# Kernel optimization log

Measured on AMD Instinct MI355X. Metric: run time of the kernel, lower is better.

## Reference

```python
import jax, jax.numpy as jnp
import numpy as np

D_MODEL = 1024
N_HEADS = 16
D_K = D_MODEL // N_HEADS
WINDOW = 512
ROPE_BASE = 10000.0


def _apply_rope(x):
    # x: [B, H, S, D] ; torchtune-style interleaved-pair RoPE
    S, D = x.shape[2], x.shape[3]
    half = D // 2
    inv_freq = 1.0 / (ROPE_BASE ** (jnp.arange(half, dtype=jnp.float32) / half))
    ang = jnp.arange(S, dtype=jnp.float32)[:, None] * inv_freq[None, :]  # [S, half]
    cos = jnp.cos(ang).astype(x.dtype)  # [S, half]
    sin = jnp.sin(ang).astype(x.dtype)
    x_even = x[..., ::2]   # [B,H,S,half]
    x_odd = x[..., 1::2]
    out_even = x_even * cos - x_odd * sin
    out_odd = x_odd * cos + x_even * sin
    return jnp.stack([out_even, out_odd], axis=-1).reshape(x.shape)


def setup_inputs() -> dict:
    key = jax.random.key(0)
    k1, k2, k3 = jax.random.split(key, 3)
    B, S = 2, 2048
    x = jax.random.normal(k1, (B, S, D_MODEL), dtype=jnp.float32)
    # store weights pre-transposed so y = x @ w (same math as nn.Linear)
    w_qkv = jax.random.normal(k2, (D_MODEL, 3 * D_MODEL), dtype=jnp.float32) * (D_MODEL ** -0.5)
    w_o = jax.random.normal(k3, (D_MODEL, D_MODEL), dtype=jnp.float32) * (D_MODEL ** -0.5)
    return {"x": x, "w_qkv": w_qkv, "w_o": w_o}


def reference(x, w_qkv, w_o):
    B, S, _ = x.shape
    qkv = (x @ w_qkv).reshape(B, S, 3, N_HEADS, D_K)
    qkv = jnp.transpose(qkv, (2, 0, 3, 1, 4))  # [3, B, H, S, Dk]
    q, k, v = qkv[0], qkv[1], qkv[2]
    q = _apply_rope(q)
    k = _apply_rope(k)
    # causal sliding-window mask: token i attends to j in [i - WINDOW, i]
    i = jnp.arange(S)[:, None]
    j = jnp.arange(S)[None, :]
    allowed = (j <= i) & (j >= i - WINDOW)
    bias = jnp.where(allowed, 0.0, -jnp.inf).astype(x.dtype)  # [S, S]
    scores = jnp.einsum('bhqd,bhkd->bhqk', q, k) * (D_K ** -0.5) + bias
    attn = jax.nn.softmax(scores, axis=-1)
    out = jnp.einsum('bhqk,bhkd->bhqd', attn, v)  # [B,H,S,Dk]
    out = jnp.transpose(out, (0, 2, 1, 3)).reshape(B, S, D_MODEL)
    return out @ w_o
```

## Files before the change

kernel.cpp:

```cpp
#include <hip/hip_runtime.h>
#include <hip/hip_bf16.h>
#include <math.h>

typedef __bf16 bhalf;
typedef __bf16 bhalf8 __attribute__((ext_vector_type(8)));
typedef float floatx4 __attribute__((ext_vector_type(4)));
typedef _Float16 fh;
typedef _Float16 half4 __attribute__((ext_vector_type(4)));

#define MFMA_BF16(A, B, C) __builtin_amdgcn_mfma_f32_16x16x32_bf16((A), (B), (C), 0, 0, 0)
#define MFMA_F16_K16(A, B, C) __builtin_amdgcn_mfma_f32_16x16x16f16((A), (B), (C), 0, 0, 0)

__device__ inline unsigned short bfb(float f) {
  union { bhalf h; unsigned short u; } c;
  c.h = (bhalf)f;
  return c.u;
}
__device__ inline unsigned short fhb(float f) {
  union { fh h; unsigned short u; } c;
  c.h = (fh)f;
  return c.u;
}

__device__ inline void gload_lds16(const void* g, void* l) {
  typedef const __attribute__((address_space(1))) unsigned int GU;
  typedef __attribute__((address_space(3))) unsigned int LU;
  __builtin_amdgcn_global_load_lds((GU*)g, (LU*)l, 16, 0, 0);
}

__global__ __launch_bounds__(256) void prep_kernel(const float* __restrict__ x,
                                                   const float* __restrict__ wqkv,
                                                   const float* __restrict__ wo,
                                                   bhalf* __restrict__ x_bf,
                                                   bhalf* __restrict__ wqkvT,
                                                   bhalf* __restrict__ woT) {
  __shared__ float tile[32][33];
  const int bx = blockIdx.x;
  if (bx < 2048) {
    int i = (bx * 256 + threadIdx.x) * 8;
    floatx4 v0 = *(const floatx4*)(x + i);
    floatx4 v1 = *(const floatx4*)(x + i + 4);
    bhalf8 o;
    o[0] = (bhalf)v0[0]; o[1] = (bhalf)v0[1]; o[2] = (bhalf)v0[2]; o[3] = (bhalf)v0[3];
    o[4] = (bhalf)v1[0]; o[5] = (bhalf)v1[1]; o[6] = (bhalf)v1[2]; o[7] = (bhalf)v1[3];
    *(bhalf8*)(x_bf + i) = o;
    return;
  }
  const float* in;
  bhalf* out;
  int C, cx, ry;
  if (bx < 5120) {
    int idx = bx - 2048;
    in = wqkv; out = wqkvT; C = 3072;
    cx = idx % 96; ry = idx / 96;
  } else {
    int idx = bx - 5120;
    in = wo; out = woT; C = 1024;
    cx = idx & 31; ry = idx >> 5;
  }
  const int R = 1024;
  int c0 = cx * 32, r0 = ry * 32;
  int tx = threadIdx.x & 31, ty = threadIdx.x >> 5;
#pragma unroll
  for (int i = 0; i < 32; i += 8)
    tile[ty + i][tx] = in[(size_t)(r0 + ty + i) * C + c0 + tx];
  __syncthreads();
#pragma unroll
  for (int i = 0; i < 32; i += 8)
    out[(size_t)(c0 + ty + i) * R + r0 + tx] = (bhalf)tile[tx][ty + i];
}

template <int EPI, int TN>
__global__ __launch_bounds__(256, 2) void gemm_bt_kernel(
    const bhalf* __restrict__ A, const bhalf* __restrict__ BT, float* __restrict__ Cout,
    bhalf* __restrict__ qb, bhalf* __restrict__ kb, fh* __restrict__ vb,
    int M, int N, int K) {
  constexpr int NT = TN / 32;
  __shared__ __attribute__((aligned(16))) bhalf As[128 * 64];
  __shared__ __attribute__((aligned(16))) bhalf Bs[TN * 64];
  const int tid = threadIdx.x;
  const int lane = tid & 63;
  const int w = tid >> 6, wr = w >> 1, wc = w & 1;
  const int m0 = blockIdx.y * 128, n0 = blockIdx.x * TN;
  const int l15 = lane & 15, lhi = lane >> 4;

  floatx4 acc[4][NT];
#pragma unroll
  for (int i = 0; i < 4; ++i)
#pragma unroll
    for (int j = 0; j < NT; ++j) acc[i][j] = (floatx4){0.f, 0.f, 0.f, 0.f};

  const int srow16 = lane >> 2;
  const int scg = (lane & 3) ^ ((lane >> 3) & 3);
  const bhalf* aP0 = A + (size_t)(m0 + 32 * w + srow16) * K + scg * 8;
  const bhalf* aP1 = aP0 + (size_t)16 * K;
  const bhalf* bP0 = BT + (size_t)(n0 + ((TN == 128) ? 32 * w : 16 * w) + srow16) * K + scg * 8;
  const bhalf* bP1 = bP0 + (size_t)16 * K;
  bhalf* aL0 = &As[(2 * w) * 512];
  bhalf* aL1 = &As[(2 * w + 1) * 512];
  bhalf* bL0 = (TN == 128) ? &Bs[(2 * w) * 512] : &Bs[w * 512];
  bhalf* bL1 = (TN == 128) ? &Bs[(2 * w + 1) * 512] : nullptr;

  const int fro = (l15 * 4 + (lhi ^ ((l15 >> 1) & 3))) * 8;

  for (int k0 = 0; k0 < K; k0 += 64) {
    __syncthreads();
    gload_lds16(aP0 + k0, aL0);
    gload_lds16(aP1 + k0, aL1);
    gload_lds16(bP0 + k0, bL0);
    if constexpr (TN == 128) gload_lds16(bP1 + k0, bL1);
    gload_lds16(aP0 + k0 + 32, aL0 + 4096);
    gload_lds16(aP1 + k0 + 32, aL1 + 4096);
    gload_lds16(bP0 + k0 + 32, bL0 + TN * 32);
    if constexpr (TN == 128) gload_lds16(bP1 + k0 + 32, bL1 + TN * 32);
    __syncthreads();
#pragma unroll
    for (int kh = 0; kh < 2; ++kh) {
      bhalf8 af[4], bf[NT];
#pragma unroll
      for (int mt = 0; mt < 4; ++mt)
        af[mt] = *(const bhalf8*)&As[kh * 4096 + (wr * 4 + mt) * 512 + fro];
#pragma unroll
      for (int nt = 0; nt < NT; ++nt)
        bf[nt] = *(const bhalf8*)&Bs[kh * TN * 32 + (wc * NT + nt) * 512 + fro];
#pragma unroll
      for (int mt = 0; mt < 4; ++mt)
#pragma unroll
        for (int nt = 0; nt < NT; ++nt)
          acc[mt][nt] = MFMA_BF16(af[mt], bf[nt], acc[mt][nt]);
    }
  }

  if constexpr (EPI == 0) {
#pragma unroll
    for (int mt = 0; mt < 4; ++mt)
#pragma unroll
      for (int nt = 0; nt < NT; ++nt)
#pragma unroll
        for (int r = 0; r < 4; ++r) {
          int mg = m0 + wr * 64 + mt * 16 + lhi * 4 + r;
          int ng = n0 + wc * (TN / 2) + nt * 16 + l15;
          Cout[(size_t)mg * N + ng] = acc[mt][nt][r];
        }
  } else {
    const int sel = n0 >> 10;
    if (sel == 2) {
#pragma unroll
      for (int mt = 0; mt < 4; ++mt) {
        int mg = m0 + wr * 64 + mt * 16 + lhi * 4;
        int b = mg >> 11, s0 = mg & 2047;
#pragma unroll
        for (int nt = 0; nt < NT; ++nt) {
          int ng = n0 + wc * (TN / 2) + nt * 16 + l15;
          int h = (ng & 1023) >> 6, d = ng & 63;
          union { unsigned short u[4]; uint2 v2; } pk;
#pragma unroll
          for (int r = 0; r < 4; ++r) pk.u[r] = fhb(acc[mt][nt][r]);
          *(uint2*)&vb[((size_t)((b << 4) + h) * 64 + d) * 2048 + s0] = pk.v2;
        }
      }
    } else {
      bhalf* dst = sel ? kb : qb;
      const float post = sel ? 1.0f : 0.18033688f;
#pragma unroll
      for (int nt = 0; nt < NT; ++nt) {
        int ng = n0 + wc * (TN / 2) + nt * 16 + l15;
        int h = (ng & 1023) >> 6, d = ng & 63;
        float inv = exp2f((float)(d >> 1) * -0.4152410118609203f);
#pragma unroll
        for (int mt = 0; mt < 4; ++mt) {
          int mg = m0 + wr * 64 + mt * 16 + lhi * 4;
          int b = mg >> 11, s0 = mg & 2047;
#pragma unroll
          for (int r = 0; r < 4; ++r) {
            float val = acc[mt][nt][r];
            float partner = __shfl_xor(val, 1, 64);
            if (!(l15 & 1)) {
              float ang = (float)(s0 + r) * inv;
              float sn = __sinf(ang), cs = __cosf(ang);
              float oe = (cs * val - sn * partner) * post;
              float oo = (cs * partner + sn * val) * post;
              unsigned int u = bfb(oe) | ((unsigned int)bfb(oo) << 16);
              *(unsigned int*)&dst[((size_t)((b << 4) + h) * 2048 + (s0 + r)) * 64 + d] = u;
            }
          }
        }
      }
    }
  }
}

__global__ __launch_bounds__(256, 3) void attn_kernel(const bhalf* __restrict__ qg,
                                                      const bhalf* __restrict__ kg,
                                                      const fh* __restrict__ vt,
                                                      bhalf* __restrict__ attn_out) {
  __shared__ __attribute__((aligned(16))) bhalf Ks[2][8 * 512];
  __shared__ __attribute__((aligned(16))) fh Vs[2][16 * 256];

  const int bh = blockIdx.x;
  const int qt2 = blockIdx.y;
  const int tid = threadIdx.x, lane = tid & 63, w = tid >> 6;
  const int l15 = lane & 15, quad = lane >> 4;
  const int q0 = qt2 * 128;
  const int qtile0 = qt2 * 2;
  const size_t base = (size_t)bh * 2048 * 64;
  const size_t vbase = (size_t)bh * 64 * 2048;

  bhalf8 qa[2][2];
#pragma unroll
  for (int h = 0; h < 2; ++h) {
    const bhalf* qp = qg + base + (size_t)(q0 + h * 64 + w * 16 + l15) * 64 + quad * 8;
    qa[h][0] = *(const bhalf8*)qp;
    qa[h][1] = *(const bhalf8*)(qp + 32);
  }

  const int kOff = (w * 16 + (lane >> 2)) * 64 + (lane & 3) * 8;
  const int vfb0 = 4 * w + (lane >> 5), vfb1 = 4 * w + 2 + (lane >> 5);
  const int vOff0 = ((vfb0 & 3) * 16 + ((lane & 31) >> 1)) * 2048 + w * 16 + (lane & 1) * 8;
  const int vOff1 = ((vfb1 & 3) * 16 + ((lane & 31) >> 1)) * 2048 + w * 16 + (lane & 1) * 8;

  floatx4 O[2][4];
#pragma unroll
  for (int h = 0; h < 2; ++h)
#pragma unroll
    for (int dt = 0; dt < 4; ++dt) O[h][dt] = (floatx4){0.f, 0.f, 0.f, 0.f};
  float lsum[2] = {0.f, 0.f};

  auto stage = [&](int kt, int buf) {
    const bhalf* kp = kg + base + (size_t)(kt * 64) * 64 + kOff;
    gload_lds16(kp, &Ks[buf][(2 * w) * 512]);
    gload_lds16(kp + 32, &Ks[buf][(2 * w + 1) * 512]);
    const fh* vp = vt + vbase + kt * 64;
    gload_lds16(vp + vOff0, &Vs[buf][(2 * w) * 512]);
    gload_lds16(vp + vOff1, &Vs[buf][(2 * w + 1) * 512]);
  };

  auto proc = [&](int buf, int kt, int h) {
    const int diag = qtile0 + h;
    if (kt > diag || kt < diag - 8) return;
    const int iG = q0 + h * 64 + w * 16 + l15;
    floatx4 sf[4];
#pragma unroll
    for (int nt = 0; nt < 4; ++nt) {
      bhalf8 k0 = *(const bhalf8*)&Ks[buf][(nt * 2) * 512 + (l15 * 4 + quad) * 8];
      bhalf8 k1 = *(const bhalf8*)&Ks[buf][(nt * 2 + 1) * 512 + (l15 * 4 + quad) * 8];
      floatx4 s = (floatx4){0.f, 0.f, 0.f, 0.f};
      s = MFMA_BF16(k0, qa[h][0], s);
      s = MFMA_BF16(k1, qa[h][1], s);
      sf[nt] = s;
    }
    if (kt == diag) {
#pragma unroll
      for (int nt = 0; nt < 4; ++nt) {
        int jb = kt * 64 + nt * 16 + quad * 4;
#pragma unroll
        for (int r = 0; r < 4; ++r)
          if (jb + r > iG) sf[nt][r] = -1e30f;
      }
    } else if (kt == diag - 8) {
#pragma unroll
      for (int nt = 0; nt < 4; ++nt) {
        int jb = kt * 64 + nt * 16 + quad * 4;
#pragma unroll
        for (int r = 0; r < 4; ++r)
          if (jb + r + 512 < iG) sf[nt][r] = -1e30f;
      }
    }
#pragma unroll
    for (int nt = 0; nt < 4; ++nt) {
      half4 pf;
#pragma unroll
      for (int r = 0; r < 4; ++r) {
        float p = exp2f(sf[nt][r]);
        lsum[h] += p;
        pf[r] = (fh)p;
      }
#pragma unroll
      for (int dt = 0; dt < 4; ++dt) {
        half4 vf = *(const half4*)&Vs[buf][(nt * 4 + dt) * 256 + (l15 * 4 + quad) * 4];
        O[h][dt] = MFMA_F16_K16(vf, pf, O[h][dt]);
      }
    }
  };

  int ktstart = qtile0 - 8;
  if (ktstart < 0) ktstart = 0;
  const int ktend = qtile0 + 1;
  for (int kt = ktstart; kt <= ktend; kt += 2) {
    __syncthreads();
    stage(kt, 0);
    stage(kt + 1, 1);
    __syncthreads();
    proc(0, kt, 0);
    proc(0, kt, 1);
    proc(1, kt + 1, 0);
    proc(1, kt + 1, 1);
  }

  const int b = bh >> 4, hh = bh & 15;
#pragma unroll
  for (int h = 0; h < 2; ++h) {
    float t = lsum[h];
    t += __shfl_xor(t, 16, 64);
    t += __shfl_xor(t, 32, 64);
    const float inv = 1.f / t;
    const int s = q0 + h * 64 + w * 16 + l15;
#pragma unroll
    for (int dt = 0; dt < 4; ++dt) {
      union { unsigned short u[4]; uint2 v2; } pk;
#pragma unroll
      for (int r = 0; r < 4; ++r) pk.u[r] = bfb(O[h][dt][r] * inv);
      *(uint2*)&attn_out[(size_t)(b * 2048 + s) * 1024 + hh * 64 + dt * 16 + quad * 4] = pk.v2;
    }
  }
}

extern "C" void kernel_launch(void* const* d_in, const int* in_sizes, int n_in,
                              void* d_out, int out_size, void* d_ws, size_t ws_size,
                              hipStream_t stream) {
  (void)in_sizes; (void)n_in; (void)out_size; (void)ws_size;
  const float* x = (const float*)d_in[0];
  const float* w_qkv = (const float*)d_in[1];
  const float* w_o = (const float*)d_in[2];
  float* out = (float*)d_out;
  char* ws = (char*)d_ws;

  bhalf* x_bf  = (bhalf*)(ws);
  bhalf* wqkvT = (bhalf*)(ws + ((size_t)8 << 20));
  bhalf* woT   = (bhalf*)(ws + ((size_t)14 << 20));
  bhalf* qb    = (bhalf*)(ws + ((size_t)16 << 20));
  bhalf* kb    = (bhalf*)(ws + ((size_t)24 << 20));
  fh*    vb    = (fh*)(ws + ((size_t)32 << 20));
  bhalf* attn  = (bhalf*)(ws + ((size_t)40 << 20));

  prep_kernel<<<6144, 256, 0, stream>>>(x, w_qkv, w_o, x_bf, wqkvT, woT);
  gemm_bt_kernel<1, 128><<<dim3(24, 32), 256, 0, stream>>>(x_bf, wqkvT, nullptr, qb, kb, vb,
                                                           4096, 3072, 1024);
  attn_kernel<<<dim3(32, 16), 256, 0, stream>>>(qb, kb, vb, attn);
  gemm_bt_kernel<0, 64><<<dim3(16, 32), 256, 0, stream>>>(attn, woT, out, nullptr, nullptr,
                                                          nullptr, 4096, 1024, 1024);
}
```

Baseline: 160.8 us.

## Software-pipeline K/V staging and merge both query halves per tile in attention

```diff
diff --git a/kernel.cpp b/kernel.cpp
--- a/kernel.cpp
+++ b/kernel.cpp
@@ -6,7 +6,9 @@
 typedef __bf16 bhalf8 __attribute__((ext_vector_type(8)));
 typedef float floatx4 __attribute__((ext_vector_type(4)));
 typedef _Float16 fh;
+typedef _Float16 half2 __attribute__((ext_vector_type(2)));
 typedef _Float16 half4 __attribute__((ext_vector_type(4)));
+typedef __fp16 fp16x2 __attribute__((ext_vector_type(2)));
 
 #define MFMA_BF16(A, B, C) __builtin_amdgcn_mfma_f32_16x16x32_bf16((A), (B), (C), 0, 0, 0)
 #define MFMA_F16_K16(A, B, C) __builtin_amdgcn_mfma_f32_16x16x16f16((A), (B), (C), 0, 0, 0)
@@ -20,6 +22,9 @@
   union { fh h; unsigned short u; } c;
   c.h = (fh)f;
   return c.u;
+}
+__device__ inline half2 cvt_pk_f16(float a, float b) {
+  return __builtin_bit_cast(half2, __builtin_amdgcn_cvt_pkrtz(a, b));
 }
 
 __device__ inline void gload_lds16(const void* g, void* l) {
@@ -190,7 +195,7 @@
   }
 }
 
-__global__ __launch_bounds__(256, 3) void attn_kernel(const bhalf* __restrict__ qg,
+__global__ __launch_bounds__(256, 2) void attn_kernel(const bhalf* __restrict__ qg,
                                                       const bhalf* __restrict__ kg,
                                                       const fh* __restrict__ vt,
                                                       bhalf* __restrict__ attn_out) {
@@ -235,66 +240,91 @@
     gload_lds16(vp + vOff1, &Vs[buf][(2 * w + 1) * 512]);
   };
 
-  auto proc = [&](int buf, int kt, int h) {
-    const int diag = qtile0 + h;
-    if (kt > diag || kt < diag - 8) return;
-    const int iG = q0 + h * 64 + w * 16 + l15;
-    floatx4 sf[4];
+  auto proc2 = [&](int buf, int kt) {
+    const bool va = (kt <= qtile0) && (kt >= qtile0 - 8);
+    const bool vb_ = (kt <= qtile0 + 1) && (kt >= qtile0 - 7);
+    floatx4 sf[2][4];
+    __builtin_amdgcn_s_setprio(1);
 #pragma unroll
     for (int nt = 0; nt < 4; ++nt) {
       bhalf8 k0 = *(const bhalf8*)&Ks[buf][(nt * 2) * 512 + (l15 * 4 + quad) * 8];
       bhalf8 k1 = *(const bhalf8*)&Ks[buf][(nt * 2 + 1) * 512 + (l15 * 4 + quad) * 8];
-      floatx4 s = (floatx4){0.f, 0.f, 0.f, 0.f};
-      s = MFMA_BF16(k0, qa[h][0], s);
-      s = MFMA_BF16(k1, qa[h][1], s);
-      sf[nt] = s;
-    }
-    if (kt == diag) {
+      floatx4 s0 = (floatx4){0.f, 0.f, 0.f, 0.f};
+      floatx4 s1 = (floatx4){0.f, 0.f, 0.f, 0.f};
+      if (va) {
+        s0 = MFMA_BF16(k0, qa[0][0], s0);
+        s0 = MFMA_BF16(k1, qa[0][1], s0);
+      }
+      if (vb_) {
+        s1 = MFMA_BF16(k0, qa[1][0], s1);
+        s1 = MFMA_BF16(k1, qa[1][1], s1);
+      }
+      sf[0][nt] = s0;
+      sf[1][nt] = s1;
+    }
+    __builtin_amdgcn_s_setprio(0);
+
+    half4 pf[2][4];
+#pragma unroll
+    for (int h = 0; h < 2; ++h) {
+      if (!(h == 0 ? va : vb_)) continue;
+      const int diag = qtile0 + h;
+      const int iG = q0 + h * 64 + w * 16 + l15;
+      if (kt == diag) {
+#pragma unroll
+        for (int nt = 0; nt < 4; ++nt) {
+          int jb = kt * 64 + nt * 16 + quad * 4;
+#pragma unroll
+          for (int r = 0; r < 4; ++r)
+            if (jb + r > iG) sf[h][nt][r] = -1e30f;
+        }
+      } else if (kt == diag - 8) {
+#pragma unroll
+        for (int nt = 0; nt < 4; ++nt) {
+          int jb = kt * 64 + nt * 16 + quad * 4;
+#pragma unroll
+          for (int r = 0; r < 4; ++r)
+            if (jb + r + 512 < iG) sf[h][nt][r] = -1e30f;
+        }
+      }
 #pragma unroll
       for (int nt = 0; nt < 4; ++nt) {
-        int jb = kt * 64 + nt * 16 + quad * 4;
-#pragma unroll
-        for (int r = 0; r < 4; ++r)
-          if (jb + r > iG) sf[nt][r] = -1e30f;
-      }
-    } else if (kt == diag - 8) {
-#pragma unroll
-      for (int nt = 0; nt < 4; ++nt) {
-        int jb = kt * 64 + nt * 16 + quad * 4;
-#pragma unroll
-        for (int r = 0; r < 4; ++r)
-          if (jb + r + 512 < iG) sf[nt][r] = -1e30f;
-      }
-    }
+        float p0 = exp2f(sf[h][nt][0]);
+        float p1 = exp2f(sf[h][nt][1]);
+        float p2 = exp2f(sf[h][nt][2]);
+        float p3 = exp2f(sf[h][nt][3]);
+        lsum[h] += (p0 + p1) + (p2 + p3);
+        union { half2 h2[2]; half4 h4; } pu;
+        pu.h2[0] = cvt_pk_f16(p0, p1);
+        pu.h2[1] = cvt_pk_f16(p2, p3);
+        pf[h][nt] = pu.h4;
+      }
+    }
+
+    __builtin_amdgcn_s_setprio(1);
 #pragma unroll
     for (int nt = 0; nt < 4; ++nt) {
-      half4 pf;
-#pragma unroll
-      for (int r = 0; r < 4; ++r) {
-        float p = exp2f(sf[nt][r]);
-        lsum[h] += p;
-        pf[r] = (fh)p;
-      }
 #pragma unroll
       for (int dt = 0; dt < 4; ++dt) {
         half4 vf = *(const half4*)&Vs[buf][(nt * 4 + dt) * 256 + (l15 * 4 + quad) * 4];
-        O[h][dt] = MFMA_F16_K16(vf, pf, O[h][dt]);
-      }
-    }
+        if (va) O[0][dt] = MFMA_F16_K16(vf, pf[0][nt], O[0][dt]);
+        if (vb_) O[1][dt] = MFMA_F16_K16(vf, pf[1][nt], O[1][dt]);
+      }
+    }
+    __builtin_amdgcn_s_setprio(0);
   };
 
   int ktstart = qtile0 - 8;
   if (ktstart < 0) ktstart = 0;
   const int ktend = qtile0 + 1;
-  for (int kt = ktstart; kt <= ktend; kt += 2) {
+
+  stage(ktstart, 0);
+  __syncthreads();
+  for (int kt = ktstart; kt <= ktend; ++kt) {
+    const int cb = (kt - ktstart) & 1;
+    if (kt < ktend) stage(kt + 1, cb ^ 1);
+    proc2(cb, kt);
     __syncthreads();
-    stage(kt, 0);
-    stage(kt + 1, 1);
-    __syncthreads();
-    proc(0, kt, 0);
-    proc(0, kt, 1);
-    proc(1, kt + 1, 0);
-    proc(1, kt + 1, 1);
   }
 
   const int b = bh >> 4, hh = bh & 15;
```

After: 161.2 us. About the same (+0.3%).

## Load K/V fragments directly from global memory in attention, one query tile per block

Applied to the files above, without the earlier changes.

```diff
diff --git a/kernel.cpp b/kernel.cpp
--- a/kernel.cpp
+++ b/kernel.cpp
@@ -6,6 +6,7 @@
 typedef __bf16 bhalf8 __attribute__((ext_vector_type(8)));
 typedef float floatx4 __attribute__((ext_vector_type(4)));
 typedef _Float16 fh;
+typedef _Float16 half2 __attribute__((ext_vector_type(2)));
 typedef _Float16 half4 __attribute__((ext_vector_type(4)));
 
 #define MFMA_BF16(A, B, C) __builtin_amdgcn_mfma_f32_16x16x32_bf16((A), (B), (C), 0, 0, 0)
@@ -20,6 +21,9 @@
   union { fh h; unsigned short u; } c;
   c.h = (fh)f;
   return c.u;
+}
+__device__ inline half2 cvt_pk_f16(float a, float b) {
+  return __builtin_bit_cast(half2, __builtin_amdgcn_cvt_pkrtz(a, b));
 }
 
 __device__ inline void gload_lds16(const void* g, void* l) {
@@ -190,66 +194,50 @@
   }
 }
 
-__global__ __launch_bounds__(256, 3) void attn_kernel(const bhalf* __restrict__ qg,
+__global__ __launch_bounds__(256, 4) void attn_kernel(const bhalf* __restrict__ qg,
                                                       const bhalf* __restrict__ kg,
                                                       const fh* __restrict__ vt,
                                                       bhalf* __restrict__ attn_out) {
-  __shared__ __attribute__((aligned(16))) bhalf Ks[2][8 * 512];
-  __shared__ __attribute__((aligned(16))) fh Vs[2][16 * 256];
-
   const int bh = blockIdx.x;
-  const int qt2 = blockIdx.y;
+  const int qt = blockIdx.y;
   const int tid = threadIdx.x, lane = tid & 63, w = tid >> 6;
   const int l15 = lane & 15, quad = lane >> 4;
-  const int q0 = qt2 * 128;
-  const int qtile0 = qt2 * 2;
+  const int q0 = qt * 64;
   const size_t base = (size_t)bh * 2048 * 64;
   const size_t vbase = (size_t)bh * 64 * 2048;
 
-  bhalf8 qa[2][2];
-#pragma unroll
-  for (int h = 0; h < 2; ++h) {
-    const bhalf* qp = qg + base + (size_t)(q0 + h * 64 + w * 16 + l15) * 64 + quad * 8;
-    qa[h][0] = *(const bhalf8*)qp;
-    qa[h][1] = *(const bhalf8*)(qp + 32);
-  }
-
-  const int kOff = (w * 16 + (lane >> 2)) * 64 + (lane & 3) * 8;
-  const int vfb0 = 4 * w + (lane >> 5), vfb1 = 4 * w + 2 + (lane >> 5);
-  const int vOff0 = ((vfb0 & 3) * 16 + ((lane & 31) >> 1)) * 2048 + w * 16 + (lane & 1) * 8;
-  const int vOff1 = ((vfb1 & 3) * 16 + ((lane & 31) >> 1)) * 2048 + w * 16 + (lane & 1) * 8;
-
-  floatx4 O[2][4];
-#pragma unroll
-  for (int h = 0; h < 2; ++h)
-#pragma unroll
-    for (int dt = 0; dt < 4; ++dt) O[h][dt] = (floatx4){0.f, 0.f, 0.f, 0.f};
-  float lsum[2] = {0.f, 0.f};
-
-  auto stage = [&](int kt, int buf) {
-    const bhalf* kp = kg + base + (size_t)(kt * 64) * 64 + kOff;
-    gload_lds16(kp, &Ks[buf][(2 * w) * 512]);
-    gload_lds16(kp + 32, &Ks[buf][(2 * w + 1) * 512]);
-    const fh* vp = vt + vbase + kt * 64;
-    gload_lds16(vp + vOff0, &Vs[buf][(2 * w) * 512]);
-    gload_lds16(vp + vOff1, &Vs[buf][(2 * w + 1) * 512]);
-  };
-
-  auto proc = [&](int buf, int kt, int h) {
-    const int diag = qtile0 + h;
-    if (kt > diag || kt < diag - 8) return;
-    const int iG = q0 + h * 64 + w * 16 + l15;
+  const bhalf* qp = qg + base + (size_t)(q0 + w * 16 + l15) * 64 + quad * 8;
+  const bhalf8 qa0 = *(const bhalf8*)qp;
+  const bhalf8 qa1 = *(const bhalf8*)(qp + 32);
+
+  const bhalf* kfrag = kg + base + (size_t)l15 * 64 + quad * 8;
+  const fh* vfrag = vt + vbase + (size_t)l15 * 2048 + quad * 4;
+  const int iG = q0 + w * 16 + l15;
+
+  floatx4 O[4];
+#pragma unroll
+  for (int dt = 0; dt < 4; ++dt) O[dt] = (floatx4){0.f, 0.f, 0.f, 0.f};
+  float lsum = 0.f;
+
+  int ktstart = qt - 8;
+  if (ktstart < 0) ktstart = 0;
+
+  for (int kt = ktstart; kt <= qt; ++kt) {
     floatx4 sf[4];
+    __builtin_amdgcn_s_setprio(1);
 #pragma unroll
     for (int nt = 0; nt < 4; ++nt) {
-      bhalf8 k0 = *(const bhalf8*)&Ks[buf][(nt * 2) * 512 + (l15 * 4 + quad) * 8];
-      bhalf8 k1 = *(const bhalf8*)&Ks[buf][(nt * 2 + 1) * 512 + (l15 * 4 + quad) * 8];
+      const bhalf* kp = kfrag + (size_t)(kt * 64 + nt * 16) * 64;
+      bhalf8 k0 = *(const bhalf8*)kp;
+      bhalf8 k1 = *(const bhalf8*)(kp + 32);
       floatx4 s = (floatx4){0.f, 0.f, 0.f, 0.f};
-      s = MFMA_BF16(k0, qa[h][0], s);
-      s = MFMA_BF16(k1, qa[h][1], s);
+      s = MFMA_BF16(k0, qa0, s);
+      s = MFMA_BF16(k1, qa1, s);
       sf[nt] = s;
     }
-    if (kt == diag) {
+    __builtin_amdgcn_s_setprio(0);
+
+    if (kt == qt) {
 #pragma unroll
       for (int nt = 0; nt < 4; ++nt) {
         int jb = kt * 64 + nt * 16 + quad * 4;
@@ -257,7 +245,7 @@
         for (int r = 0; r < 4; ++r)
           if (jb + r > iG) sf[nt][r] = -1e30f;
       }
-    } else if (kt == diag - 8) {
+    } else if (kt == qt - 8) {
 #pragma unroll
       for (int nt = 0; nt < 4; ++nt) {
         int jb = kt * 64 + nt * 16 + quad * 4;
@@ -266,52 +254,46 @@
           if (jb + r + 512 < iG) sf[nt][r] = -1e30f;
       }
     }
+
+    half4 pf[4];
 #pragma unroll
     for (int nt = 0; nt < 4; ++nt) {
-      half4 pf;
-#pragma unroll
-      for (int r = 0; r < 4; ++r) {
-        float p = exp2f(sf[nt][r]);
-        lsum[h] += p;
-        pf[r] = (fh)p;
-      }
+      float p0 = exp2f(sf[nt][0]);
+      float p1 = exp2f(sf[nt][1]);
+      float p2 = exp2f(sf[nt][2]);
+      float p3 = exp2f(sf[nt][3]);
+      lsum += (p0 + p1) + (p2 + p3);
+      union { half2 h2[2]; half4 h4; } pu;
+      pu.h2[0] = cvt_pk_f16(p0, p1);
+      pu.h2[1] = cvt_pk_f16(p2, p3);
+      pf[nt] = pu.h4;
+    }
+
+    __builtin_amdgcn_s_setprio(1);
+#pragma unroll
+    for (int nt = 0; nt < 4; ++nt) {
+      const fh* vp = vfrag + kt * 64 + nt * 16;
 #pragma unroll
       for (int dt = 0; dt < 4; ++dt) {
-        half4 vf = *(const half4*)&Vs[buf][(nt * 4 + dt) * 256 + (l15 * 4 + quad) * 4];
-        O[h][dt] = MFMA_F16_K16(vf, pf, O[h][dt]);
-      }
-    }
-  };
-
-  int ktstart = qtile0 - 8;
-  if (ktstart < 0) ktstart = 0;
-  const int ktend = qtile0 + 1;
-  for (int kt = ktstart; kt <= ktend; kt += 2) {
-    __syncthreads();
-    stage(kt, 0);
-    stage(kt + 1, 1);
-    __syncthreads();
-    proc(0, kt, 0);
-    proc(0, kt, 1);
-    proc(1, kt + 1, 0);
-    proc(1, kt + 1, 1);
-  }
-
+        half4 vf = *(const half4*)&vp[(size_t)(dt * 16) * 2048];
+        O[dt] = MFMA_F16_K16(vf, pf[nt], O[dt]);
+      }
+    }
+    __builtin_amdgcn_s_setprio(0);
+  }
+
+  float t = lsum;
+  t += __shfl_xor(t, 16, 64);
+  t += __shfl_xor(t, 32, 64);
+  const float inv = 1.f / t;
   const int b = bh >> 4, hh = bh & 15;
-#pragma unroll
-  for (int h = 0; h < 2; ++h) {
-    float t = lsum[h];
-    t += __shfl_xor(t, 16, 64);
-    t += __shfl_xor(t, 32, 64);
-    const float inv = 1.f / t;
-    const int s = q0 + h * 64 + w * 16 + l15;
-#pragma unroll
-    for (int dt = 0; dt < 4; ++dt) {
-      union { unsigned short u[4]; uint2 v2; } pk;
-#pragma unroll
-      for (int r = 0; r < 4; ++r) pk.u[r] = bfb(O[h][dt][r] * inv);
-      *(uint2*)&attn_out[(size_t)(b * 2048 + s) * 1024 + hh * 64 + dt * 16 + quad * 4] = pk.v2;
-    }
+  const int s = q0 + w * 16 + l15;
+#pragma unroll
+  for (int dt = 0; dt < 4; ++dt) {
+    union { unsigned short u[4]; uint2 v2; } pk;
+#pragma unroll
+    for (int r = 0; r < 4; ++r) pk.u[r] = bfb(O[dt][r] * inv);
+    *(uint2*)&attn_out[(size_t)(b * 2048 + s) * 1024 + hh * 64 + dt * 16 + quad * 4] = pk.v2;
   }
 }
 
@@ -336,7 +318,7 @@
   prep_kernel<<<6144, 256, 0, stream>>>(x, w_qkv, w_o, x_bf, wqkvT, woT);
   gemm_bt_kernel<1, 128><<<dim3(24, 32), 256, 0, stream>>>(x_bf, wqkvT, nullptr, qb, kb, vb,
                                                            4096, 3072, 1024);
-  attn_kernel<<<dim3(32, 16), 256, 0, stream>>>(qb, kb, vb, attn);
+  attn_kernel<<<dim3(32, 32), 256, 0, stream>>>(qb, kb, vb, attn);
   gemm_bt_kernel<0, 64><<<dim3(16, 32), 256, 0, stream>>>(attn, woT, out, nullptr, nullptr,
                                                           nullptr, 4096, 1024, 1024);
 }
```

Result: slower. 227.0 us (+41.2%).
